# Performance work log

Hardware: AMD Instinct MI355X
Metric: run time of the kernel (lower is better)

Reference implementation:

```python
import jax, jax.numpy as jnp
import numpy as np
from jax import lax

B, C, H, T = 128, 64, 32, 256


def _xavier(key, shape):
    fan_out, fan_in = shape[-2], shape[-1]
    s = np.sqrt(6.0 / (fan_in + fan_out)).astype(np.float32)
    return jax.random.uniform(key, shape, jnp.float32, -s, s)


def setup_inputs() -> dict:
    key = jax.random.key(0)
    ks = jax.random.split(key, 12)
    x = jax.random.normal(ks[0], (B, C, T), jnp.float32)
    m = jax.random.uniform(ks[1], (B, C, T), jnp.float32)
    d = jax.random.uniform(ks[2], (B, C, T), jnp.float32)
    Wf = _xavier(ks[3], (C, H, H))
    Vf = _xavier(ks[4], (C, H, 3))
    cf = _xavier(ks[5], (C, H, 1))[:, :, 0]          # (C, H)
    Wb = _xavier(ks[6], (C, H, H))
    Vb = _xavier(ks[7], (C, H, 3))
    cb = _xavier(ks[8], (C, H, 1))[:, :, 0]          # (C, H)
    U = _xavier(ks[9], (C, 1, 2 * H))[:, 0, :]        # (C, 2H)
    c0 = 0.1 * jax.random.normal(ks[10], (C,), jnp.float32)
    return {"x": x, "m": m, "d": d, "Wf": Wf, "Vf": Vf, "cf": cf,
            "Wb": Wb, "Vb": Vb, "cb": cb, "U": U, "c0": c0}


def _mrnn(x, m, d, Wf, Vf, cf, Wb, Vb, cb, U, c0):
    act = jax.nn.relu
    Tn = x.shape[-1]
    pad = lambda a: jnp.pad(a, ((0, 0), (0, 0), (1, 1)), mode="edge")  # replication pad
    feats = jnp.stack([pad(x), pad(m), pad(d)], axis=-1)   # (B, C, T+2, 3)
    # forward RNN sees padded times 0..T-1 (orig t-1); backward sees padded T+1..2 (orig t+1)
    in_f = jnp.transpose(feats[:, :, :Tn], (2, 0, 1, 3))               # (T, B, C, 3)
    in_b = jnp.transpose(feats[:, :, 2:Tn + 2][:, :, ::-1], (2, 0, 1, 3))

    def scan_rnn(W, V, c, inp):
        def step(h, v):
            # per-channel block-diagonal matmul: batched tiny GEMM over C
            hn = act(jnp.einsum("chk,bck->bch", W, h)
                     + jnp.einsum("chj,bcj->bch", V, v) + c)
            return hn, hn
        h0 = jnp.zeros((x.shape[0], W.shape[0], W.shape[1]), x.dtype)
        return lax.scan(step, h0, inp)[1]                  # (T, B, C, H)

    hf = scan_rnn(Wf, Vf, cf, in_f)
    hb = scan_rnn(Wb, Vb, cb, in_b)[::-1]                  # align backward states with t
    hcat = jnp.concatenate([hf, hb], axis=-1)              # (T, B, C, 2H)
    out = act(jnp.einsum("ck,tbck->tbc", U, hcat) + c0)    # (T, B, C)
    return jnp.transpose(out, (1, 2, 0))                   # (B, C, T)


def reference(x, m, d, Wf, Vf, cf, Wb, Vb, cb, U, c0):
    return _mrnn(x, m, d, Wf, Vf, cf, Wb, Vb, cb, U, c0)
```

## Files before the change

### kernel.cpp

```cpp
#include <hip/hip_runtime.h>

constexpr int Bn = 128, Cn = 64, Hn = 32, Tn = 256;

typedef __attribute__((ext_vector_type(8))) short short8;
typedef __attribute__((ext_vector_type(4))) float f32x4;
typedef __attribute__((ext_vector_type(4))) unsigned int u32x4;

__device__ __forceinline__ unsigned pk_hi(unsigned y, unsigned x) {
  return __builtin_amdgcn_perm(y, x, 0x07060302u);
}

__device__ __forceinline__ void wsplit(float w, short& hi, short& lo) {
  unsigned u = __float_as_uint(w);
  float r = w - __uint_as_float(u & 0xffff0000u);
  unsigned ru = __float_as_uint(r) + 0x8000u;
  hi = (short)(u >> 16);
  lo = (short)(ru >> 16);
}

__global__ __launch_bounds__(64, 1)
void mrnn_scan(const float* __restrict__ x, const float* __restrict__ m,
               const float* __restrict__ d,
               const float* __restrict__ Wf, const float* __restrict__ Vf,
               const float* __restrict__ cf,
               const float* __restrict__ Wb, const float* __restrict__ Vb,
               const float* __restrict__ cb,
               const float* __restrict__ U,
               float* __restrict__ pf_out, float* __restrict__ pb_out) {
  const int bid = blockIdx.x;
  const int dir = bid >> 9;
  const int c   = (bid >> 3) & (Cn - 1);
  const int g   = bid & 7;
  const int tid = threadIdx.x;
  const int q = tid >> 4;
  const int n = tid & 15;
  const int b = g * 16 + n;

  const float* W  = dir ? Wb : Wf;
  const float* V  = dir ? Vb : Vf;
  const float* cc = dir ? cb : cf;

  const int ra0 = 8 * (n >> 2) + (n & 3);
  const int ra1 = ra0 + 4;
  short8 A0h, A0l, A1h, A1l;
#pragma unroll
  for (int j = 0; j < 8; ++j) {
    short hi, lo;
    wsplit(W[(c * Hn + ra0) * Hn + 8 * q + j], hi, lo); A0h[j] = hi; A0l[j] = lo;
    wsplit(W[(c * Hn + ra1) * Hn + 8 * q + j], hi, lo); A1h[j] = hi; A1l[j] = lo;
  }

  float v0x[4], v0y[4], v0z[4], bs0[4], uu0[4];
  float v1x[4], v1y[4], v1z[4], bs1[4], uu1[4];
#pragma unroll
  for (int r = 0; r < 4; ++r) {
    const int row0 = 8 * q + r, row1 = row0 + 4;
    const float* vp0 = V + (c * Hn + row0) * 3;
    v0x[r] = vp0[0]; v0y[r] = vp0[1]; v0z[r] = vp0[2];
    bs0[r] = cc[c * Hn + row0];
    uu0[r] = U[c * 2 * Hn + dir * Hn + row0];
    const float* vp1 = V + (c * Hn + row1) * 3;
    v1x[r] = vp1[0]; v1y[r] = vp1[1]; v1z[r] = vp1[2];
    bs1[r] = cc[c * Hn + row1];
    uu1[r] = U[c * 2 * Hn + dir * Hn + row1];
  }

  u32x4 Bh = {0u, 0u, 0u, 0u};
  u32x4 Bl = {0u, 0u, 0u, 0u};

  const long base = ((long)b * Cn + c) * Tn;
  const float* px = x + base;
  const float* pm = m + base;
  const float* pd = d + base;
  float* pout = (dir ? pb_out : pf_out) + base;

  float cx, cm2, cd2;
  f32x4 qx, qm, qd;
  if (!dir) {
    cx = px[0]; cm2 = pm[0]; cd2 = pd[0];
    qx = *(const f32x4*)px; qm = *(const f32x4*)pm; qd = *(const f32x4*)pd;
  } else {
    cx = px[Tn - 1]; cm2 = pm[Tn - 1]; cd2 = pd[Tn - 1];
    qx = *(const f32x4*)(px + Tn - 4);
    qm = *(const f32x4*)(pm + Tn - 4);
    qd = *(const f32x4*)(pd + Tn - 4);
  }

  for (int t0 = 0; t0 < Tn; t0 += 4) {
    int qn_ = dir ? (Tn - 8 - t0) : (t0 + 4);
    if (qn_ < 0) qn_ = 0;
    if (qn_ > Tn - 4) qn_ = Tn - 4;
    const f32x4 nqx = *(const f32x4*)(px + qn_);
    const f32x4 nqm = *(const f32x4*)(pm + qn_);
    const f32x4 nqd = *(const f32x4*)(pd + qn_);

    float inx[4], inm[4], ind[4];
    if (!dir) {
      inx[0] = cx;  inx[1] = qx.x; inx[2] = qx.y; inx[3] = qx.z;
      inm[0] = cm2; inm[1] = qm.x; inm[2] = qm.y; inm[3] = qm.z;
      ind[0] = cd2; ind[1] = qd.x; ind[2] = qd.y; ind[3] = qd.z;
      cx = qx.w; cm2 = qm.w; cd2 = qd.w;
    } else {
      inx[0] = cx;  inx[1] = qx.w; inx[2] = qx.z; inx[3] = qx.y;
      inm[0] = cm2; inm[1] = qm.w; inm[2] = qm.z; inm[3] = qm.y;
      ind[0] = cd2; ind[1] = qd.w; ind[2] = qd.z; ind[3] = qd.y;
      cx = qx.x; cm2 = qm.x; cd2 = qd.x;
    }

    f32x4 pacc;
#pragma unroll
    for (int u = 0; u < 4; ++u) {
      const float ix = inx[u], im = inm[u], idv = ind[u];
      f32x4 acc0, acc1;
#pragma unroll
      for (int r = 0; r < 4; ++r) {
        acc0[r] = fmaf(v0x[r], ix, fmaf(v0y[r], im, fmaf(v0z[r], idv, bs0[r])));
        acc1[r] = fmaf(v1x[r], ix, fmaf(v1y[r], im, fmaf(v1z[r], idv, bs1[r])));
      }
      const short8 bh = __builtin_bit_cast(short8, Bh);
      const short8 bl = __builtin_bit_cast(short8, Bl);
      acc0 = __builtin_amdgcn_mfma_f32_16x16x32_bf16(A0l, bh, acc0, 0, 0, 0);
      acc1 = __builtin_amdgcn_mfma_f32_16x16x32_bf16(A1l, bh, acc1, 0, 0, 0);
      acc0 = __builtin_amdgcn_mfma_f32_16x16x32_bf16(A0h, bl, acc0, 0, 0, 0);
      acc1 = __builtin_amdgcn_mfma_f32_16x16x32_bf16(A1h, bl, acc1, 0, 0, 0);
      acc0 = __builtin_amdgcn_mfma_f32_16x16x32_bf16(A0h, bh, acc0, 0, 0, 0);
      acc1 = __builtin_amdgcn_mfma_f32_16x16x32_bf16(A1h, bh, acc1, 0, 0, 0);
#pragma unroll
      for (int r = 0; r < 4; ++r) {
        acc0[r] = fmaxf(acc0[r], 0.f);
        acc1[r] = fmaxf(acc1[r], 0.f);
      }
      float p = uu0[0] * acc0[0];
      p = fmaf(uu0[1], acc0[1], p); p = fmaf(uu0[2], acc0[2], p);
      p = fmaf(uu0[3], acc0[3], p);
      p = fmaf(uu1[0], acc1[0], p); p = fmaf(uu1[1], acc1[1], p);
      p = fmaf(uu1[2], acc1[2], p); p = fmaf(uu1[3], acc1[3], p);
      pacc[u] = p;
      const unsigned h00 = __float_as_uint(acc0[0]), h01 = __float_as_uint(acc0[1]);
      const unsigned h02 = __float_as_uint(acc0[2]), h03 = __float_as_uint(acc0[3]);
      const unsigned h10 = __float_as_uint(acc1[0]), h11 = __float_as_uint(acc1[1]);
      const unsigned h12 = __float_as_uint(acc1[2]), h13 = __float_as_uint(acc1[3]);
      Bh[0] = pk_hi(h01, h00); Bh[1] = pk_hi(h03, h02);
      Bh[2] = pk_hi(h11, h10); Bh[3] = pk_hi(h13, h12);
      unsigned ru[8];
#pragma unroll
      for (int r = 0; r < 4; ++r) {
        ru[r]     = __float_as_uint(acc0[r] - __uint_as_float(__float_as_uint(acc0[r]) & 0xffff0000u)) + 0x8000u;
        ru[4 + r] = __float_as_uint(acc1[r] - __uint_as_float(__float_as_uint(acc1[r]) & 0xffff0000u)) + 0x8000u;
      }
      Bl[0] = pk_hi(ru[1], ru[0]); Bl[1] = pk_hi(ru[3], ru[2]);
      Bl[2] = pk_hi(ru[5], ru[4]); Bl[3] = pk_hi(ru[7], ru[6]);
    }
#pragma unroll
    for (int u = 0; u < 4; ++u) pacc[u] += __shfl_xor(pacc[u], 16);
#pragma unroll
    for (int u = 0; u < 4; ++u) pacc[u] += __shfl_xor(pacc[u], 32);

    if (q == 0) {
      if (!dir) {
        *(f32x4*)(pout + t0) = pacc;
      } else {
        f32x4 rev = {pacc[3], pacc[2], pacc[1], pacc[0]};
        *(f32x4*)(pout + (Tn - 4 - t0)) = rev;
      }
    }
    qx = nqx; qm = nqm; qd = nqd;
  }
}

__global__ __launch_bounds__(256)
void mrnn_combine(const float* __restrict__ pb, const float* __restrict__ c0,
                  float* __restrict__ out) {
  const int i4 = blockIdx.x * 256 + threadIdx.x;
  const int c = (i4 >> 6) & (Cn - 1);
  const float c0v = c0[c];
  float4 a = ((const float4*)out)[i4];
  const float4 bb = ((const float4*)pb)[i4];
  a.x = fmaxf(a.x + bb.x + c0v, 0.f);
  a.y = fmaxf(a.y + bb.y + c0v, 0.f);
  a.z = fmaxf(a.z + bb.z + c0v, 0.f);
  a.w = fmaxf(a.w + bb.w + c0v, 0.f);
  ((float4*)out)[i4] = a;
}

extern "C" void kernel_launch(void* const* d_in, const int* in_sizes, int n_in,
                              void* d_out, int out_size, void* d_ws, size_t ws_size,
                              hipStream_t stream) {
  const float* x  = (const float*)d_in[0];
  const float* m  = (const float*)d_in[1];
  const float* dd = (const float*)d_in[2];
  const float* Wf = (const float*)d_in[3];
  const float* Vf = (const float*)d_in[4];
  const float* cf = (const float*)d_in[5];
  const float* Wb = (const float*)d_in[6];
  const float* Vb = (const float*)d_in[7];
  const float* cb = (const float*)d_in[8];
  const float* U  = (const float*)d_in[9];
  const float* c0 = (const float*)d_in[10];
  float* out = (float*)d_out;
  float* pb  = (float*)d_ws;

  mrnn_scan<<<1024, 64, 0, stream>>>(x, m, dd, Wf, Vf, cf, Wb, Vb, cb, U, out, pb);
  mrnn_combine<<<(Bn * Cn * Tn) / (256 * 4), 256, 0, stream>>>(pb, c0, out);
}
```

Measured before the change: 157.8 us.

## Split each recurrence across two waves exchanging hidden state through LDS

Each block now runs two waves, each computing half of the hidden rows (one MFMA chain instead of two). The wave halves exchange their bf16 hi/lo packed states through double-buffered shared memory with a block barrier every timestep, and partial output projections are summed through LDS. This is meant to shorten the per-step serial MFMA dependency chain by spreading it across waves. In exchange it adds a __syncthreads and LDS round trip on every recurrent step, which sits on the critical path.

```diff
diff --git a/kernel.cpp b/kernel.cpp
--- a/kernel.cpp
+++ b/kernel.cpp
@@ -5,6 +5,7 @@
 typedef __attribute__((ext_vector_type(8))) short short8;
 typedef __attribute__((ext_vector_type(4))) float f32x4;
 typedef __attribute__((ext_vector_type(4))) unsigned int u32x4;
+typedef __attribute__((ext_vector_type(2))) unsigned int u32x2;
 
 __device__ __forceinline__ unsigned pk_hi(unsigned y, unsigned x) {
   return __builtin_amdgcn_perm(y, x, 0x07060302u);
@@ -18,7 +19,7 @@
   lo = (short)(ru >> 16);
 }
 
-__global__ __launch_bounds__(64, 1)
+__global__ __launch_bounds__(128)
 void mrnn_scan(const float* __restrict__ x, const float* __restrict__ m,
                const float* __restrict__ d,
                const float* __restrict__ Wf, const float* __restrict__ Vf,
@@ -32,37 +33,36 @@
   const int c   = (bid >> 3) & (Cn - 1);
   const int g   = bid & 7;
   const int tid = threadIdx.x;
-  const int q = tid >> 4;
-  const int n = tid & 15;
+  const int wave = tid >> 6;
+  const int lane = tid & 63;
+  const int q = lane >> 4;
+  const int n = lane & 15;
   const int b = g * 16 + n;
+
+  __shared__ __align__(16) unsigned exs[2][64 * 12];
+  __shared__ __align__(16) float pbuf[16][4];
 
   const float* W  = dir ? Wb : Wf;
   const float* V  = dir ? Vb : Vf;
   const float* cc = dir ? cb : cf;
 
-  const int ra0 = 8 * (n >> 2) + (n & 3);
-  const int ra1 = ra0 + 4;
-  short8 A0h, A0l, A1h, A1l;
+  const int ra = 8 * (n >> 2) + (n & 3) + wave * 4;
+  short8 Ah, Al;
 #pragma unroll
   for (int j = 0; j < 8; ++j) {
     short hi, lo;
-    wsplit(W[(c * Hn + ra0) * Hn + 8 * q + j], hi, lo); A0h[j] = hi; A0l[j] = lo;
-    wsplit(W[(c * Hn + ra1) * Hn + 8 * q + j], hi, lo); A1h[j] = hi; A1l[j] = lo;
-  }
-
-  float v0x[4], v0y[4], v0z[4], bs0[4], uu0[4];
-  float v1x[4], v1y[4], v1z[4], bs1[4], uu1[4];
+    wsplit(W[(c * Hn + ra) * Hn + 8 * q + j], hi, lo);
+    Ah[j] = hi; Al[j] = lo;
+  }
+
+  float vx[4], vy[4], vz[4], bs[4], uu[4];
 #pragma unroll
   for (int r = 0; r < 4; ++r) {
-    const int row0 = 8 * q + r, row1 = row0 + 4;
-    const float* vp0 = V + (c * Hn + row0) * 3;
-    v0x[r] = vp0[0]; v0y[r] = vp0[1]; v0z[r] = vp0[2];
-    bs0[r] = cc[c * Hn + row0];
-    uu0[r] = U[c * 2 * Hn + dir * Hn + row0];
-    const float* vp1 = V + (c * Hn + row1) * 3;
-    v1x[r] = vp1[0]; v1y[r] = vp1[1]; v1z[r] = vp1[2];
-    bs1[r] = cc[c * Hn + row1];
-    uu1[r] = U[c * 2 * Hn + dir * Hn + row1];
+    const int row = 8 * q + wave * 4 + r;
+    const float* vp = V + (c * Hn + row) * 3;
+    vx[r] = vp[0]; vy[r] = vp[1]; vz[r] = vp[2];
+    bs[r] = cc[c * Hn + row];
+    uu[r] = U[c * 2 * Hn + dir * Hn + row];
   }
 
   u32x4 Bh = {0u, 0u, 0u, 0u};
@@ -85,6 +85,9 @@
     qm = *(const f32x4*)(pm + Tn - 4);
     qd = *(const f32x4*)(pd + Tn - 4);
   }
+
+  unsigned* rec0 = &exs[0][lane * 12];
+  unsigned* rec1 = &exs[1][lane * 12];
 
   for (int t0 = 0; t0 < Tn; t0 += 4) {
     int qn_ = dir ? (Tn - 8 - t0) : (t0 + 4);
@@ -110,57 +113,57 @@
     f32x4 pacc;
 #pragma unroll
     for (int u = 0; u < 4; ++u) {
+      unsigned* rec = (u & 1) ? rec1 : rec0;
       const float ix = inx[u], im = inm[u], idv = ind[u];
-      f32x4 acc0, acc1;
-#pragma unroll
-      for (int r = 0; r < 4; ++r) {
-        acc0[r] = fmaf(v0x[r], ix, fmaf(v0y[r], im, fmaf(v0z[r], idv, bs0[r])));
-        acc1[r] = fmaf(v1x[r], ix, fmaf(v1y[r], im, fmaf(v1z[r], idv, bs1[r])));
-      }
+      f32x4 acc;
+#pragma unroll
+      for (int r = 0; r < 4; ++r)
+        acc[r] = fmaf(vx[r], ix, fmaf(vy[r], im, fmaf(vz[r], idv, bs[r])));
       const short8 bh = __builtin_bit_cast(short8, Bh);
       const short8 bl = __builtin_bit_cast(short8, Bl);
-      acc0 = __builtin_amdgcn_mfma_f32_16x16x32_bf16(A0l, bh, acc0, 0, 0, 0);
-      acc1 = __builtin_amdgcn_mfma_f32_16x16x32_bf16(A1l, bh, acc1, 0, 0, 0);
-      acc0 = __builtin_amdgcn_mfma_f32_16x16x32_bf16(A0h, bl, acc0, 0, 0, 0);
-      acc1 = __builtin_amdgcn_mfma_f32_16x16x32_bf16(A1h, bl, acc1, 0, 0, 0);
-      acc0 = __builtin_amdgcn_mfma_f32_16x16x32_bf16(A0h, bh, acc0, 0, 0, 0);
-      acc1 = __builtin_amdgcn_mfma_f32_16x16x32_bf16(A1h, bh, acc1, 0, 0, 0);
-#pragma unroll
-      for (int r = 0; r < 4; ++r) {
-        acc0[r] = fmaxf(acc0[r], 0.f);
-        acc1[r] = fmaxf(acc1[r], 0.f);
-      }
-      float p = uu0[0] * acc0[0];
-      p = fmaf(uu0[1], acc0[1], p); p = fmaf(uu0[2], acc0[2], p);
-      p = fmaf(uu0[3], acc0[3], p);
-      p = fmaf(uu1[0], acc1[0], p); p = fmaf(uu1[1], acc1[1], p);
-      p = fmaf(uu1[2], acc1[2], p); p = fmaf(uu1[3], acc1[3], p);
+      acc = __builtin_amdgcn_mfma_f32_16x16x32_bf16(Al, bh, acc, 0, 0, 0);
+      acc = __builtin_amdgcn_mfma_f32_16x16x32_bf16(Ah, bl, acc, 0, 0, 0);
+      acc = __builtin_amdgcn_mfma_f32_16x16x32_bf16(Ah, bh, acc, 0, 0, 0);
+#pragma unroll
+      for (int r = 0; r < 4; ++r) acc[r] = fmaxf(acc[r], 0.f);
+
+      float p = uu[0] * acc[0];
+      p = fmaf(uu[1], acc[1], p); p = fmaf(uu[2], acc[2], p);
+      p = fmaf(uu[3], acc[3], p);
       pacc[u] = p;
-      const unsigned h00 = __float_as_uint(acc0[0]), h01 = __float_as_uint(acc0[1]);
-      const unsigned h02 = __float_as_uint(acc0[2]), h03 = __float_as_uint(acc0[3]);
-      const unsigned h10 = __float_as_uint(acc1[0]), h11 = __float_as_uint(acc1[1]);
-      const unsigned h12 = __float_as_uint(acc1[2]), h13 = __float_as_uint(acc1[3]);
-      Bh[0] = pk_hi(h01, h00); Bh[1] = pk_hi(h03, h02);
-      Bh[2] = pk_hi(h11, h10); Bh[3] = pk_hi(h13, h12);
-      unsigned ru[8];
-#pragma unroll
-      for (int r = 0; r < 4; ++r) {
-        ru[r]     = __float_as_uint(acc0[r] - __uint_as_float(__float_as_uint(acc0[r]) & 0xffff0000u)) + 0x8000u;
-        ru[4 + r] = __float_as_uint(acc1[r] - __uint_as_float(__float_as_uint(acc1[r]) & 0xffff0000u)) + 0x8000u;
-      }
-      Bl[0] = pk_hi(ru[1], ru[0]); Bl[1] = pk_hi(ru[3], ru[2]);
-      Bl[2] = pk_hi(ru[5], ru[4]); Bl[3] = pk_hi(ru[7], ru[6]);
+
+      const unsigned h0 = __float_as_uint(acc[0]), h1 = __float_as_uint(acc[1]);
+      const unsigned h2 = __float_as_uint(acc[2]), h3 = __float_as_uint(acc[3]);
+      const unsigned oh0 = pk_hi(h1, h0), oh1 = pk_hi(h3, h2);
+      unsigned ru[4];
+#pragma unroll
+      for (int r = 0; r < 4; ++r)
+        ru[r] = __float_as_uint(acc[r] -
+                 __uint_as_float(__float_as_uint(acc[r]) & 0xffff0000u)) + 0x8000u;
+      const unsigned ol0 = pk_hi(ru[1], ru[0]), ol1 = pk_hi(ru[3], ru[2]);
+
+      *(u32x2*)(rec + 2 * wave)     = (u32x2){oh0, oh1};
+      *(u32x2*)(rec + 4 + 2 * wave) = (u32x2){ol0, ol1};
+      __syncthreads();
+      Bh = *(const u32x4*)rec;
+      Bl = *(const u32x4*)(rec + 4);
     }
 #pragma unroll
     for (int u = 0; u < 4; ++u) pacc[u] += __shfl_xor(pacc[u], 16);
 #pragma unroll
     for (int u = 0; u < 4; ++u) pacc[u] += __shfl_xor(pacc[u], 32);
 
-    if (q == 0) {
+    if (wave == 1 && q == 0) *(f32x4*)pbuf[n] = pacc;
+    __syncthreads();
+    if (wave == 0 && q == 0) {
+      const f32x4 o = *(const f32x4*)pbuf[n];
       if (!dir) {
-        *(f32x4*)(pout + t0) = pacc;
+        f32x4 s = {pacc[0] + o[0], pacc[1] + o[1],
+                   pacc[2] + o[2], pacc[3] + o[3]};
+        *(f32x4*)(pout + t0) = s;
       } else {
-        f32x4 rev = {pacc[3], pacc[2], pacc[1], pacc[0]};
+        f32x4 rev = {pacc[3] + o[3], pacc[2] + o[2],
+                     pacc[1] + o[1], pacc[0] + o[0]};
         *(f32x4*)(pout + (Tn - 4 - t0)) = rev;
       }
     }
@@ -200,6 +203,6 @@
   float* out = (float*)d_out;
   float* pb  = (float*)d_ws;
 
-  mrnn_scan<<<1024, 64, 0, stream>>>(x, m, dd, Wf, Vf, cf, Wb, Vb, cb, U, out, pb);
+  mrnn_scan<<<1024, 128, 0, stream>>>(x, m, dd, Wf, Vf, cf, Wb, Vb, cb, U, out, pb);
   mrnn_combine<<<(Bn * Cn * Tn) / (256 * 4), 256, 0, stream>>>(pb, c0, out);
 }
```

Result: slower. 181.7 us (+15.1%).

## Split MFMA dependency chain into parallel accumulators and unroll time by eight

Applied to the files above, without the earlier changes.

Each recurrent step's three chained bf16 MFMAs per tile are split into two independent chains, the hi×hi product into a zero accumulator and the correction terms into the input-projection accumulator, then summed before the ReLU. This shortens the serial MFMA latency on the recurrence's critical path. The time loop is also unrolled from 4 to 8 steps with 8-wide input prefetch and output stores, cutting per-iteration loop and shuffle overhead at the cost of more registers. Summation order changes slightly.

```diff
diff --git a/kernel.cpp b/kernel.cpp
--- a/kernel.cpp
+++ b/kernel.cpp
@@ -67,6 +67,7 @@
 
   u32x4 Bh = {0u, 0u, 0u, 0u};
   u32x4 Bl = {0u, 0u, 0u, 0u};
+  const f32x4 z4 = {0.f, 0.f, 0.f, 0.f};
 
   const long base = ((long)b * Cn + c) * Tn;
   const float* px = x + base;
@@ -75,60 +76,69 @@
   float* pout = (dir ? pb_out : pf_out) + base;
 
   float cx, cm2, cd2;
-  f32x4 qx, qm, qd;
+  f32x4 qx0, qx1, qm0, qm1, qd0, qd1;
   if (!dir) {
     cx = px[0]; cm2 = pm[0]; cd2 = pd[0];
-    qx = *(const f32x4*)px; qm = *(const f32x4*)pm; qd = *(const f32x4*)pd;
+    qx0 = *(const f32x4*)px;        qx1 = *(const f32x4*)(px + 4);
+    qm0 = *(const f32x4*)pm;        qm1 = *(const f32x4*)(pm + 4);
+    qd0 = *(const f32x4*)pd;        qd1 = *(const f32x4*)(pd + 4);
   } else {
     cx = px[Tn - 1]; cm2 = pm[Tn - 1]; cd2 = pd[Tn - 1];
-    qx = *(const f32x4*)(px + Tn - 4);
-    qm = *(const f32x4*)(pm + Tn - 4);
-    qd = *(const f32x4*)(pd + Tn - 4);
-  }
-
-  for (int t0 = 0; t0 < Tn; t0 += 4) {
-    int qn_ = dir ? (Tn - 8 - t0) : (t0 + 4);
+    qx0 = *(const f32x4*)(px + Tn - 8); qx1 = *(const f32x4*)(px + Tn - 4);
+    qm0 = *(const f32x4*)(pm + Tn - 8); qm1 = *(const f32x4*)(pm + Tn - 4);
+    qd0 = *(const f32x4*)(pd + Tn - 8); qd1 = *(const f32x4*)(pd + Tn - 4);
+  }
+
+  for (int t0 = 0; t0 < Tn; t0 += 8) {
+    int qn_ = dir ? (Tn - 16 - t0) : (t0 + 8);
     if (qn_ < 0) qn_ = 0;
-    if (qn_ > Tn - 4) qn_ = Tn - 4;
-    const f32x4 nqx = *(const f32x4*)(px + qn_);
-    const f32x4 nqm = *(const f32x4*)(pm + qn_);
-    const f32x4 nqd = *(const f32x4*)(pd + qn_);
-
-    float inx[4], inm[4], ind[4];
+    if (qn_ > Tn - 8) qn_ = Tn - 8;
+    const f32x4 nx0 = *(const f32x4*)(px + qn_), nx1 = *(const f32x4*)(px + qn_ + 4);
+    const f32x4 nm0 = *(const f32x4*)(pm + qn_), nm1 = *(const f32x4*)(pm + qn_ + 4);
+    const f32x4 nd0 = *(const f32x4*)(pd + qn_), nd1 = *(const f32x4*)(pd + qn_ + 4);
+
+    float vxa[8] = {qx0.x, qx0.y, qx0.z, qx0.w, qx1.x, qx1.y, qx1.z, qx1.w};
+    float vma[8] = {qm0.x, qm0.y, qm0.z, qm0.w, qm1.x, qm1.y, qm1.z, qm1.w};
+    float vda[8] = {qd0.x, qd0.y, qd0.z, qd0.w, qd1.x, qd1.y, qd1.z, qd1.w};
+    float inx[8], inm[8], ind[8];
+    inx[0] = cx; inm[0] = cm2; ind[0] = cd2;
     if (!dir) {
-      inx[0] = cx;  inx[1] = qx.x; inx[2] = qx.y; inx[3] = qx.z;
-      inm[0] = cm2; inm[1] = qm.x; inm[2] = qm.y; inm[3] = qm.z;
-      ind[0] = cd2; ind[1] = qd.x; ind[2] = qd.y; ind[3] = qd.z;
-      cx = qx.w; cm2 = qm.w; cd2 = qd.w;
+#pragma unroll
+      for (int k = 1; k < 8; ++k) {
+        inx[k] = vxa[k - 1]; inm[k] = vma[k - 1]; ind[k] = vda[k - 1];
+      }
+      cx = vxa[7]; cm2 = vma[7]; cd2 = vda[7];
     } else {
-      inx[0] = cx;  inx[1] = qx.w; inx[2] = qx.z; inx[3] = qx.y;
-      inm[0] = cm2; inm[1] = qm.w; inm[2] = qm.z; inm[3] = qm.y;
-      ind[0] = cd2; ind[1] = qd.w; ind[2] = qd.z; ind[3] = qd.y;
-      cx = qx.x; cm2 = qm.x; cd2 = qd.x;
+#pragma unroll
+      for (int k = 1; k < 8; ++k) {
+        inx[k] = vxa[8 - k]; inm[k] = vma[8 - k]; ind[k] = vda[8 - k];
+      }
+      cx = vxa[0]; cm2 = vma[0]; cd2 = vda[0];
     }
 
-    f32x4 pacc;
-#pragma unroll
-    for (int u = 0; u < 4; ++u) {
+    float pacc[8];
+#pragma unroll
+    for (int u = 0; u < 8; ++u) {
       const float ix = inx[u], im = inm[u], idv = ind[u];
-      f32x4 acc0, acc1;
+      f32x4 vi0, vi1;
 #pragma unroll
       for (int r = 0; r < 4; ++r) {
-        acc0[r] = fmaf(v0x[r], ix, fmaf(v0y[r], im, fmaf(v0z[r], idv, bs0[r])));
-        acc1[r] = fmaf(v1x[r], ix, fmaf(v1y[r], im, fmaf(v1z[r], idv, bs1[r])));
+        vi0[r] = fmaf(v0x[r], ix, fmaf(v0y[r], im, fmaf(v0z[r], idv, bs0[r])));
+        vi1[r] = fmaf(v1x[r], ix, fmaf(v1y[r], im, fmaf(v1z[r], idv, bs1[r])));
       }
       const short8 bh = __builtin_bit_cast(short8, Bh);
       const short8 bl = __builtin_bit_cast(short8, Bl);
-      acc0 = __builtin_amdgcn_mfma_f32_16x16x32_bf16(A0l, bh, acc0, 0, 0, 0);
-      acc1 = __builtin_amdgcn_mfma_f32_16x16x32_bf16(A1l, bh, acc1, 0, 0, 0);
-      acc0 = __builtin_amdgcn_mfma_f32_16x16x32_bf16(A0h, bl, acc0, 0, 0, 0);
-      acc1 = __builtin_amdgcn_mfma_f32_16x16x32_bf16(A1h, bl, acc1, 0, 0, 0);
-      acc0 = __builtin_amdgcn_mfma_f32_16x16x32_bf16(A0h, bh, acc0, 0, 0, 0);
-      acc1 = __builtin_amdgcn_mfma_f32_16x16x32_bf16(A1h, bh, acc1, 0, 0, 0);
+      f32x4 s0 = __builtin_amdgcn_mfma_f32_16x16x32_bf16(A0l, bh, vi0, 0, 0, 0);
+      f32x4 s1 = __builtin_amdgcn_mfma_f32_16x16x32_bf16(A1l, bh, vi1, 0, 0, 0);
+      f32x4 a0 = __builtin_amdgcn_mfma_f32_16x16x32_bf16(A0h, bh, z4, 0, 0, 0);
+      f32x4 a1 = __builtin_amdgcn_mfma_f32_16x16x32_bf16(A1h, bh, z4, 0, 0, 0);
+      s0 = __builtin_amdgcn_mfma_f32_16x16x32_bf16(A0h, bl, s0, 0, 0, 0);
+      s1 = __builtin_amdgcn_mfma_f32_16x16x32_bf16(A1h, bl, s1, 0, 0, 0);
+      f32x4 acc0, acc1;
 #pragma unroll
       for (int r = 0; r < 4; ++r) {
-        acc0[r] = fmaxf(acc0[r], 0.f);
-        acc1[r] = fmaxf(acc1[r], 0.f);
+        acc0[r] = fmaxf(a0[r] + s0[r], 0.f);
+        acc1[r] = fmaxf(a1[r] + s1[r], 0.f);
       }
       float p = uu0[0] * acc0[0];
       p = fmaf(uu0[1], acc0[1], p); p = fmaf(uu0[2], acc0[2], p);
@@ -152,19 +162,24 @@
       Bl[2] = pk_hi(ru[5], ru[4]); Bl[3] = pk_hi(ru[7], ru[6]);
     }
 #pragma unroll
-    for (int u = 0; u < 4; ++u) pacc[u] += __shfl_xor(pacc[u], 16);
-#pragma unroll
-    for (int u = 0; u < 4; ++u) pacc[u] += __shfl_xor(pacc[u], 32);
+    for (int u = 0; u < 8; ++u) pacc[u] += __shfl_xor(pacc[u], 16);
+#pragma unroll
+    for (int u = 0; u < 8; ++u) pacc[u] += __shfl_xor(pacc[u], 32);
 
     if (q == 0) {
       if (!dir) {
-        *(f32x4*)(pout + t0) = pacc;
+        f32x4 o0 = {pacc[0], pacc[1], pacc[2], pacc[3]};
+        f32x4 o1 = {pacc[4], pacc[5], pacc[6], pacc[7]};
+        *(f32x4*)(pout + t0) = o0;
+        *(f32x4*)(pout + t0 + 4) = o1;
       } else {
-        f32x4 rev = {pacc[3], pacc[2], pacc[1], pacc[0]};
-        *(f32x4*)(pout + (Tn - 4 - t0)) = rev;
+        f32x4 o0 = {pacc[7], pacc[6], pacc[5], pacc[4]};
+        f32x4 o1 = {pacc[3], pacc[2], pacc[1], pacc[0]};
+        *(f32x4*)(pout + (Tn - 8 - t0)) = o0;
+        *(f32x4*)(pout + (Tn - 4 - t0)) = o1;
       }
     }
-    qx = nqx; qm = nqm; qd = nqd;
+    qx0 = nx0; qx1 = nx1; qm0 = nm0; qm1 = nm1; qd0 = nd0; qd1 = nd1;
   }
 }
 
```

Measured after the change: 154.4 us. 1.02x faster.
